# Kernel optimization log

Hardware: AMD Instinct MI355X
Metric: run time of the kernel (lower is better)

Reference implementation:

```python
import jax, jax.numpy as jnp
import numpy as np

IN_F = 4096
OUT_F = 4096

def setup_inputs() -> dict:
    key = jax.random.key(0)
    k1, k2 = jax.random.split(key)
    x = jax.random.normal(k1, (4, 2048, IN_F), dtype=jnp.float32)
    W = jax.random.normal(k2, (OUT_F, IN_F), dtype=jnp.float32) * (1.0 / np.sqrt(IN_F))
    return {"x": x, "W": W}

def reference(x, W):
    # per-tensor scale = mean |W|, clamped
    scale = jnp.maximum(jnp.mean(jnp.abs(W)), 1e-8)
    # pentanet: 5-level quantization {-2,-1,0,1,2}
    w_quant = jnp.clip(jnp.round(W / scale), -2.0, 2.0)
    # STE: forward uses quantized weights, gradient flows to W
    w_ste = jax.lax.stop_gradient(w_quant * scale - W) + W
    # F.linear: x @ w_ste.T -> [b, s, out]
    return jnp.einsum('bsi,oi->bso', x, w_ste)
```

## Files before the change

kernel.cpp:

```cpp
#include <hip/hip_runtime.h>
#include <cstdint>
#include <cstddef>

#define IN_F 4096
#define OUT_F 4096

typedef __attribute__((ext_vector_type(8))) short bf16x8;
typedef __attribute__((ext_vector_type(4))) float f32x4;

__device__ __forceinline__ ushort f32_bf16_rne(float f) {
    uint32_t u = __builtin_bit_cast(uint32_t, f);
    uint32_t r = (u + 0x7FFFu + ((u >> 16) & 1u)) >> 16;
    return (ushort)r;
}

__device__ __forceinline__ void gload_lds16(const void* g, void* l) {
    __builtin_amdgcn_global_load_lds(
        (const __attribute__((address_space(1))) uint32_t*)g,
        (__attribute__((address_space(3))) uint32_t*)l,
        16, 0, 0);
}

__device__ __forceinline__ void bar() {
    asm volatile("s_barrier" ::: "memory");
}

__global__ void reduce_abs1(const float* __restrict__ W, float* __restrict__ part) {
    __shared__ float sm[256];
    const int b = blockIdx.x, t = threadIdx.x;
    const float* p = W + (size_t)b * 4096;
    float s = 0.f;
#pragma unroll
    for (int j = 0; j < 16; ++j) s += fabsf(p[t + 256 * j]);
    sm[t] = s;
    __syncthreads();
    for (int w = 128; w > 0; w >>= 1) {
        if (t < w) sm[t] += sm[t + w];
        __syncthreads();
    }
    if (t == 0) part[b] = sm[0];
}

__global__ void reduce_abs2(const float* __restrict__ part, float* __restrict__ scale) {
    __shared__ float sm[256];
    const int t = threadIdx.x;
    float s = 0.f;
#pragma unroll
    for (int j = 0; j < 16; ++j) s += part[t + 256 * j];
    sm[t] = s;
    __syncthreads();
    for (int w = 128; w > 0; w >>= 1) {
        if (t < w) sm[t] += sm[t + w];
        __syncthreads();
    }
    if (t == 0) {
        float m = sm[0] / 16777216.0f;
        *scale = fmaxf(m, 1e-8f);
    }
}

__global__ void quantize_w(const float* __restrict__ W, ushort* __restrict__ wq,
                           const float* __restrict__ scale_p) {
    const int i = blockIdx.x * 256 + threadIdx.x;
    const float s = *scale_p;
    float4 v = ((const float4*)W)[i];
    float q0 = fminf(fmaxf(rintf(v.x / s), -2.f), 2.f);
    float q1 = fminf(fmaxf(rintf(v.y / s), -2.f), 2.f);
    float q2 = fminf(fmaxf(rintf(v.z / s), -2.f), 2.f);
    float q3 = fminf(fmaxf(rintf(v.w / s), -2.f), 2.f);
    ushort4 o;
    o.x = f32_bf16_rne(q0); o.y = f32_bf16_rne(q1);
    o.z = f32_bf16_rne(q2); o.w = f32_bf16_rne(q3);
    ((ushort4*)wq)[i] = o;
}

__global__ void cast_x(const float* __restrict__ X, ushort* __restrict__ xh) {
    const int i = blockIdx.x * 256 + threadIdx.x;
    float4 v = ((const float4*)X)[i];
    ushort4 o;
    o.x = f32_bf16_rne(v.x); o.y = f32_bf16_rne(v.y);
    o.z = f32_bf16_rne(v.z); o.w = f32_bf16_rne(v.w);
    ((ushort4*)xh)[i] = o;
}

#define BK 64
#define HT_BYTES 16384
#define BUF_BYTES 65536

__global__ __launch_bounds__(512, 2) void qgemm256(
        const ushort* __restrict__ Ab, const ushort* __restrict__ Bq,
        float* __restrict__ C, const float* __restrict__ scale_p,
        int M, int N, int K) {
    extern __shared__ __align__(16) char smem[];

    const int t = threadIdx.x;
    const int lane = t & 63;
    const int w = t >> 6;
    const int wr = w >> 2;
    const int wc = w & 3;
    const int bh = wc >> 1;

    const int MT = M >> 8;
    const int NTiles = N >> 8;
    int mt, nt;
    if (MT == 32 && NTiles == 16 && gridDim.x == 512) {
        const int x = blockIdx.x & 7;
        const int j = blockIdx.x >> 3;
        const int jr = j & 31;
        const int r = j >> 5;
        mt = (x & 3) * 8 + (jr & 7);
        nt = r * 8 + (x >> 2) * 4 + (jr >> 3);
    } else {
        const int nwg = gridDim.x;
        int wg = blockIdx.x;
        if ((nwg & 7) == 0) wg = (wg & 7) * (nwg >> 3) + (wg >> 3);
        mt = wg % MT; nt = wg / MT;
    }
    const int m0 = mt << 8;
    const int n0 = nt << 8;

    const int NT = K / BK;
    const int NS = NT * 4;

    int pre[2];
#pragma unroll
    for (int ks = 0; ks < 2; ++ks)
        pre[ks] = (lane & 15) * 128 +
                  (((ks * 64) + ((lane >> 4) * 16)) ^ ((lane & 7) << 4));

    auto do_stage = [&](int s) {
        if (s >= NS) return;
        const int kt = s >> 2, h = s & 3;
        const int k0 = kt * BK;
        char* bufbase = smem + (kt & 1) * BUF_BYTES;
        char* region;
        const ushort* gsrc;
        if (h < 2) {
            region = bufbase + h * HT_BYTES;
            gsrc = Ab + (size_t)(m0 + h * 128) * K + k0;
        } else {
            region = bufbase + 32768 + (h - 2) * HT_BYTES;
            gsrc = Bq + (size_t)(n0 + (h - 2) * 128) * K + k0;
        }
#pragma unroll
        for (int j = 0; j < 2; ++j) {
            int e = j * 4096 + t * 8;
            int r = e >> 6, c8 = (e >> 3) & 7;
            int srcc = (c8 ^ (r & 7)) * 8;
            gload_lds16(gsrc + (size_t)r * K + srcc, region + e * 2);
        }
    };

    f32x4 acc[8][4];
#pragma unroll
    for (int m = 0; m < 8; ++m)
#pragma unroll
        for (int n = 0; n < 4; ++n) acc[m][n] = (f32x4){0.f, 0.f, 0.f, 0.f};

    bf16x8 a0[4][2], a1[4][2], b01[2][2], b23[2][2];

    do_stage(0); do_stage(1); do_stage(2); do_stage(3);
    do_stage(4); do_stage(5); do_stage(6);
    asm volatile("s_waitcnt vmcnt(6)" ::: "memory");
    bar();
    {
        const char* aB = smem + wr * HT_BYTES;
        const char* bB = smem + 32768 + bh * HT_BYTES + (wc & 1) * 8192;
#pragma unroll
        for (int m = 0; m < 4; ++m)
#pragma unroll
            for (int ks = 0; ks < 2; ++ks)
                a0[m][ks] = *(const bf16x8*)(aB + m * 2048 + pre[ks]);
#pragma unroll
        for (int n = 0; n < 2; ++n)
#pragma unroll
            for (int ks = 0; ks < 2; ++ks)
                b01[n][ks] = *(const bf16x8*)(bB + n * 2048 + pre[ks]);
    }

    for (int kt = 0; kt < NT; ++kt) {
        const char* aB = smem + (kt & 1) * BUF_BYTES + wr * HT_BYTES;
        const char* bB = smem + (kt & 1) * BUF_BYTES + 32768 + bh * HT_BYTES +
                         (wc & 1) * 8192;
        const char* aBn = smem + ((kt + 1) & 1) * BUF_BYTES + wr * HT_BYTES;
        const char* bBn = smem + ((kt + 1) & 1) * BUF_BYTES + 32768 +
                          bh * HT_BYTES + (wc & 1) * 8192;

        do_stage(7 + 4 * kt);
        bar();
        __builtin_amdgcn_s_setprio(1);
#pragma unroll
        for (int m = 0; m < 4; ++m)
#pragma unroll
            for (int ks = 0; ks < 2; ++ks)
                a1[m][ks] = *(const bf16x8*)(aB + (m + 4) * 2048 + pre[ks]);
#pragma unroll
        for (int m = 0; m < 4; ++m)
#pragma unroll
            for (int n = 0; n < 2; ++n)
#pragma unroll
                for (int ks = 0; ks < 2; ++ks)
                    acc[m][n] = __builtin_amdgcn_mfma_f32_16x16x32_bf16(
                        a0[m][ks], b01[n][ks], acc[m][n], 0, 0, 0);
        __builtin_amdgcn_s_setprio(0);
        bar();

        do_stage(8 + 4 * kt);
        bar();
        __builtin_amdgcn_s_setprio(1);
#pragma unroll
        for (int n = 0; n < 2; ++n)
#pragma unroll
            for (int ks = 0; ks < 2; ++ks)
                b23[n][ks] = *(const bf16x8*)(bB + (n + 2) * 2048 + pre[ks]);
#pragma unroll
        for (int m = 0; m < 4; ++m)
#pragma unroll
            for (int n = 0; n < 2; ++n)
#pragma unroll
                for (int ks = 0; ks < 2; ++ks)
                    acc[m + 4][n] = __builtin_amdgcn_mfma_f32_16x16x32_bf16(
                        a1[m][ks], b01[n][ks], acc[m + 4][n], 0, 0, 0);
        __builtin_amdgcn_s_setprio(0);
        bar();

        do_stage(9 + 4 * kt);
        bar();
        __builtin_amdgcn_s_setprio(1);
#pragma unroll
        for (int m = 0; m < 4; ++m)
#pragma unroll
            for (int n = 0; n < 2; ++n)
#pragma unroll
                for (int ks = 0; ks < 2; ++ks)
                    acc[m][n + 2] = __builtin_amdgcn_mfma_f32_16x16x32_bf16(
                        a0[m][ks], b23[n][ks], acc[m][n + 2], 0, 0, 0);
        __builtin_amdgcn_s_setprio(0);
        bar();

        if (kt < NT - 2) {
            asm volatile("s_waitcnt vmcnt(4)" ::: "memory");
        } else {
            asm volatile("s_waitcnt vmcnt(0)" ::: "memory");
        }
        do_stage(10 + 4 * kt);
        bar();
        __builtin_amdgcn_s_setprio(1);
        if (kt + 1 < NT) {
#pragma unroll
            for (int m = 0; m < 4; ++m)
#pragma unroll
                for (int ks = 0; ks < 2; ++ks)
                    a0[m][ks] = *(const bf16x8*)(aBn + m * 2048 + pre[ks]);
#pragma unroll
            for (int n = 0; n < 2; ++n)
#pragma unroll
                for (int ks = 0; ks < 2; ++ks)
                    b01[n][ks] = *(const bf16x8*)(bBn + n * 2048 + pre[ks]);
        }
#pragma unroll
        for (int m = 0; m < 4; ++m)
#pragma unroll
            for (int n = 0; n < 2; ++n)
#pragma unroll
                for (int ks = 0; ks < 2; ++ks)
                    acc[m + 4][n + 2] = __builtin_amdgcn_mfma_f32_16x16x32_bf16(
                        a1[m][ks], b23[n][ks], acc[m + 4][n + 2], 0, 0, 0);
        __builtin_amdgcn_s_setprio(0);
        bar();
    }

    const float s = *scale_p;
#pragma unroll
    for (int m = 0; m < 8; ++m)
#pragma unroll
        for (int n = 0; n < 4; ++n) {
            const int col = n0 + wc * 64 + n * 16 + (lane & 15);
            const int rbase = m0 + wr * 128 + m * 16 + ((lane >> 4) << 2);
#pragma unroll
            for (int j = 0; j < 4; ++j)
                C[(size_t)(rbase + j) * N + col] = s * acc[m][n][j];
        }
}

template <bool ABF16>
__global__ __launch_bounds__(256) void qgemm(const void* __restrict__ Aptr,
                                             const ushort* __restrict__ Bq,
                                             float* __restrict__ C,
                                             const float* __restrict__ scale_p,
                                             int M, int N, int K) {
    __shared__ __align__(16) ushort sA[128 * 64];
    __shared__ __align__(16) ushort sB[128 * 64];

    const int t = threadIdx.x;
    const int lane = t & 63;
    const int w = t >> 6;
    const int wr = w >> 1, wc = w & 1;

    const int nwg = gridDim.x;
    int wg = blockIdx.x;
    if ((nwg & 7) == 0) wg = (wg & 7) * (nwg >> 3) + (wg >> 3);
    const int MT = M >> 7;
    const int mt = wg % MT;
    const int nt = wg / MT;
    const int m0 = mt * 128, n0 = nt * 128;

    const ushort* Ab = (const ushort*)Aptr;
    const float* Af = (const float*)Aptr;

    f32x4 zero = {0.f, 0.f, 0.f, 0.f};
    f32x4 acc[4][4];
#pragma unroll
    for (int m = 0; m < 4; ++m)
#pragma unroll
        for (int n = 0; n < 4; ++n) acc[m][n] = zero;

    for (int k0 = 0; k0 < K; k0 += 64) {
#pragma unroll
        for (int i = 0; i < 4; ++i) {
            int e = i * 2048 + t * 8;
            int r = e >> 6, c8 = (e >> 3) & 7;
            int srcc = (c8 ^ (r & 7)) * 8;
            gload_lds16(Bq + (size_t)(n0 + r) * K + (k0 + srcc), &sB[e]);
        }
        if constexpr (ABF16) {
#pragma unroll
            for (int i = 0; i < 4; ++i) {
                int e = i * 2048 + t * 8;
                int r = e >> 6, c8 = (e >> 3) & 7;
                int srcc = (c8 ^ (r & 7)) * 8;
                gload_lds16(Ab + (size_t)(m0 + r) * K + (k0 + srcc), &sA[e]);
            }
        } else {
#pragma unroll
            for (int i = 0; i < 4; ++i) {
                int e = i * 2048 + t * 8;
                int r = e >> 6, c = e & 63;
                const float* src = Af + (size_t)(m0 + r) * K + (k0 + c);
                float4 v0 = *(const float4*)src;
                float4 v1 = *(const float4*)(src + 4);
                bf16x8 pk;
                pk[0] = (short)f32_bf16_rne(v0.x); pk[1] = (short)f32_bf16_rne(v0.y);
                pk[2] = (short)f32_bf16_rne(v0.z); pk[3] = (short)f32_bf16_rne(v0.w);
                pk[4] = (short)f32_bf16_rne(v1.x); pk[5] = (short)f32_bf16_rne(v1.y);
                pk[6] = (short)f32_bf16_rne(v1.z); pk[7] = (short)f32_bf16_rne(v1.w);
                int byte = (r * 128 + c * 2) ^ ((r & 7) << 4);
                *(bf16x8*)((char*)sA + byte) = pk;
            }
        }
        __syncthreads();

#pragma unroll
        for (int ks = 0; ks < 2; ++ks) {
            const int kk = ks * 32 + ((lane >> 4) << 3);
            bf16x8 afr[4], bfr[4];
#pragma unroll
            for (int m = 0; m < 4; ++m) {
                int r = wr * 64 + m * 16 + (lane & 15);
                int byte = (r * 128 + kk * 2) ^ ((r & 7) << 4);
                afr[m] = *(const bf16x8*)((const char*)sA + byte);
            }
#pragma unroll
            for (int n = 0; n < 4; ++n) {
                int r = wc * 64 + n * 16 + (lane & 15);
                int byte = (r * 128 + kk * 2) ^ ((r & 7) << 4);
                bfr[n] = *(const bf16x8*)((const char*)sB + byte);
            }
#pragma unroll
            for (int m = 0; m < 4; ++m)
#pragma unroll
                for (int n = 0; n < 4; ++n)
                    acc[m][n] = __builtin_amdgcn_mfma_f32_16x16x32_bf16(
                        afr[m], bfr[n], acc[m][n], 0, 0, 0);
        }
        __syncthreads();
    }

    const float s = *scale_p;
#pragma unroll
    for (int m = 0; m < 4; ++m)
#pragma unroll
        for (int n = 0; n < 4; ++n) {
            const int col = n0 + wc * 64 + n * 16 + (lane & 15);
            const int rbase = m0 + wr * 64 + m * 16 + ((lane >> 4) << 2);
#pragma unroll
            for (int j = 0; j < 4; ++j)
                C[(size_t)(rbase + j) * N + col] = s * acc[m][n][j];
        }
}

__global__ void naive_qgemm(const float* __restrict__ X, const float* __restrict__ W,
                            float* __restrict__ out, const float* __restrict__ scale_p,
                            int M) {
    const int col = blockIdx.x * 256 + threadIdx.x;
    const int row = blockIdx.y;
    const float s = *scale_p;
    const float inv = 1.0f / s;
    const float* xr = X + (size_t)row * IN_F;
    const float* wrow = W + (size_t)col * IN_F;
    float acc = 0.f;
    for (int k = 0; k < IN_F; ++k) {
        float q = fminf(fmaxf(rintf(wrow[k] * inv), -2.f), 2.f);
        acc += xr[k] * q;
    }
    out[(size_t)row * OUT_F + col] = acc * s;
}

extern "C" void kernel_launch(void* const* d_in, const int* in_sizes, int n_in,
                              void* d_out, int out_size, void* d_ws, size_t ws_size,
                              hipStream_t stream) {
    const float* x = (const float*)d_in[0];
    const float* W = (const float*)d_in[1];
    float* out = (float*)d_out;
    const int M = in_sizes[0] / IN_F;
    const int K = IN_F, N = OUT_F;

    char* ws = (char*)d_ws;
    const size_t OFF_PART = 512;
    const size_t OFF_WQ = OFF_PART + 4096 * sizeof(float);
    const size_t WQ_BYTES = (size_t)N * K * sizeof(ushort);
    const size_t OFF_XH = OFF_WQ + WQ_BYTES;
    const size_t XH_BYTES = (size_t)M * K * sizeof(ushort);
    float* scale = (float*)(ws + 0);
    float* part = (float*)(ws + OFF_PART);
    ushort* wq = (ushort*)(ws + OFF_WQ);
    ushort* xh = (ushort*)(ws + OFF_XH);

    if (ws_size < OFF_WQ) return;

    reduce_abs1<<<4096, 256, 0, stream>>>(W, part);
    reduce_abs2<<<1, 256, 0, stream>>>(part, scale);

    if (ws_size >= OFF_XH + XH_BYTES && (M % 256) == 0 && (N % 256) == 0) {
        quantize_w<<<(N * K / 4) / 256, 256, 0, stream>>>(W, wq, scale);
        cast_x<<<(M * K / 4) / 256, 256, 0, stream>>>(x, xh);
        (void)hipFuncSetAttribute((const void*)qgemm256,
                                  hipFuncAttributeMaxDynamicSharedMemorySize,
                                  131072);
        qgemm256<<<(M / 256) * (N / 256), 512, 131072, stream>>>(
            xh, wq, out, scale, M, N, K);
    } else if (ws_size >= OFF_XH + XH_BYTES) {
        quantize_w<<<(N * K / 4) / 256, 256, 0, stream>>>(W, wq, scale);
        cast_x<<<(M * K / 4) / 256, 256, 0, stream>>>(x, xh);
        qgemm<true><<<(M / 128) * (N / 128), 256, 0, stream>>>(xh, wq, out, scale, M, N, K);
    } else if (ws_size >= OFF_WQ + WQ_BYTES) {
        quantize_w<<<(N * K / 4) / 256, 256, 0, stream>>>(W, wq, scale);
        qgemm<false><<<(M / 128) * (N / 128), 256, 0, stream>>>(x, wq, out, scale, M, N, K);
    } else {
        naive_qgemm<<<dim3(N / 256, M), 256, 0, stream>>>(x, W, out, scale, M);
    }
}
```

Measured before the change: 328.6 us.

## Collapse four-phase GEMM pipeline into one load stage per k-tile

```diff
diff --git a/kernel.cpp b/kernel.cpp
--- a/kernel.cpp
+++ b/kernel.cpp
@@ -84,7 +84,6 @@
 }
 
 #define BK 64
-#define HT_BYTES 16384
 #define BUF_BYTES 65536
 
 __global__ __launch_bounds__(512, 2) void qgemm256(
@@ -120,7 +119,6 @@
     const int n0 = nt << 8;
 
     const int NT = K / BK;
-    const int NS = NT * 4;
 
     int pre[2];
 #pragma unroll
@@ -128,28 +126,32 @@
         pre[ks] = (lane & 15) * 128 +
                   (((ks * 64) + ((lane >> 4) * 16)) ^ ((lane & 7) << 4));
 
-    auto do_stage = [&](int s) {
-        if (s >= NS) return;
-        const int kt = s >> 2, h = s & 3;
-        const int k0 = kt * BK;
-        char* bufbase = smem + (kt & 1) * BUF_BYTES;
-        char* region;
-        const ushort* gsrc;
-        if (h < 2) {
-            region = bufbase + h * HT_BYTES;
-            gsrc = Ab + (size_t)(m0 + h * 128) * K + k0;
-        } else {
-            region = bufbase + 32768 + (h - 2) * HT_BYTES;
-            gsrc = Bq + (size_t)(n0 + (h - 2) * 128) * K + k0;
-        }
-#pragma unroll
-        for (int j = 0; j < 2; ++j) {
-            int e = j * 4096 + t * 8;
-            int r = e >> 6, c8 = (e >> 3) & 7;
-            int srcc = (c8 ^ (r & 7)) * 8;
-            gload_lds16(gsrc + (size_t)r * K + srcc, region + e * 2);
-        }
+    const int rowA = t >> 3;
+    const int colsw = ((t & 7) ^ ((t >> 3) & 7)) << 3;
+    const ushort* gA0 = Ab + (size_t)(m0 + rowA) * K + colsw;
+    const ushort* gA1 = Ab + (size_t)(m0 + 128 + rowA) * K + colsw;
+    const ushort* gB0 = Bq + (size_t)(n0 + rowA) * K + colsw;
+    const ushort* gB1 = Bq + (size_t)(n0 + 128 + rowA) * K + colsw;
+    const size_t jrow = (size_t)64 * K;
+    char* lb = smem + t * 16;
+
+    auto stA = [&](uint32_t par) {
+        gload_lds16(gA0,        lb + par);
+        gload_lds16(gA0 + jrow, lb + par + 8192);
+        gload_lds16(gA1,        lb + par + 16384);
+        gload_lds16(gA1 + jrow, lb + par + 24576);
+        gA0 += 64; gA1 += 64;
     };
+    auto stB = [&](uint32_t par) {
+        gload_lds16(gB0,        lb + par + 32768);
+        gload_lds16(gB0 + jrow, lb + par + 40960);
+        gload_lds16(gB1,        lb + par + 49152);
+        gload_lds16(gB1 + jrow, lb + par + 57344);
+        gB0 += 64; gB1 += 64;
+    };
+
+    const char* aBbase = smem + wr * 16384;
+    const char* bBbase = smem + 32768 + bh * 16384 + (wc & 1) * 8192;
 
     f32x4 acc[8][4];
 #pragma unroll
@@ -159,41 +161,36 @@
 
     bf16x8 a0[4][2], a1[4][2], b01[2][2], b23[2][2];
 
-    do_stage(0); do_stage(1); do_stage(2); do_stage(3);
-    do_stage(4); do_stage(5); do_stage(6);
-    asm volatile("s_waitcnt vmcnt(6)" ::: "memory");
+    stA(0); stB(0);
+    stA(BUF_BYTES); stB(BUF_BYTES);
+    asm volatile("s_waitcnt vmcnt(8)" ::: "memory");
     bar();
-    {
-        const char* aB = smem + wr * HT_BYTES;
-        const char* bB = smem + 32768 + bh * HT_BYTES + (wc & 1) * 8192;
-#pragma unroll
-        for (int m = 0; m < 4; ++m)
-#pragma unroll
-            for (int ks = 0; ks < 2; ++ks)
-                a0[m][ks] = *(const bf16x8*)(aB + m * 2048 + pre[ks]);
-#pragma unroll
-        for (int n = 0; n < 2; ++n)
-#pragma unroll
-            for (int ks = 0; ks < 2; ++ks)
-                b01[n][ks] = *(const bf16x8*)(bB + n * 2048 + pre[ks]);
-    }
+#pragma unroll
+    for (int m = 0; m < 4; ++m)
+#pragma unroll
+        for (int ks = 0; ks < 2; ++ks) {
+            a0[m][ks] = *(const bf16x8*)(aBbase + m * 2048 + pre[ks]);
+            a1[m][ks] = *(const bf16x8*)(aBbase + (m + 4) * 2048 + pre[ks]);
+        }
+#pragma unroll
+    for (int n = 0; n < 2; ++n)
+#pragma unroll
+        for (int ks = 0; ks < 2; ++ks) {
+            b01[n][ks] = *(const bf16x8*)(bBbase + n * 2048 + pre[ks]);
+            b23[n][ks] = *(const bf16x8*)(bBbase + (n + 2) * 2048 + pre[ks]);
+        }
 
     for (int kt = 0; kt < NT; ++kt) {
-        const char* aB = smem + (kt & 1) * BUF_BYTES + wr * HT_BYTES;
-        const char* bB = smem + (kt & 1) * BUF_BYTES + 32768 + bh * HT_BYTES +
-                         (wc & 1) * 8192;
-        const char* aBn = smem + ((kt + 1) & 1) * BUF_BYTES + wr * HT_BYTES;
-        const char* bBn = smem + ((kt + 1) & 1) * BUF_BYTES + 32768 +
-                          bh * HT_BYTES + (wc & 1) * 8192;
-
-        do_stage(7 + 4 * kt);
+        const uint32_t cur = (uint32_t)(kt & 1) * BUF_BYTES;
+        const uint32_t nxt = cur ^ BUF_BYTES;
+        const char* aBn = aBbase + nxt;
+        const char* bBn = bBbase + nxt;
+
+        asm volatile("s_waitcnt vmcnt(0)" ::: "memory");
+        if (kt + 2 < NT) { stA(cur); stB(cur); }
         bar();
+
         __builtin_amdgcn_s_setprio(1);
-#pragma unroll
-        for (int m = 0; m < 4; ++m)
-#pragma unroll
-            for (int ks = 0; ks < 2; ++ks)
-                a1[m][ks] = *(const bf16x8*)(aB + (m + 4) * 2048 + pre[ks]);
 #pragma unroll
         for (int m = 0; m < 4; ++m)
 #pragma unroll
@@ -202,17 +199,6 @@
                 for (int ks = 0; ks < 2; ++ks)
                     acc[m][n] = __builtin_amdgcn_mfma_f32_16x16x32_bf16(
                         a0[m][ks], b01[n][ks], acc[m][n], 0, 0, 0);
-        __builtin_amdgcn_s_setprio(0);
-        bar();
-
-        do_stage(8 + 4 * kt);
-        bar();
-        __builtin_amdgcn_s_setprio(1);
-#pragma unroll
-        for (int n = 0; n < 2; ++n)
-#pragma unroll
-            for (int ks = 0; ks < 2; ++ks)
-                b23[n][ks] = *(const bf16x8*)(bB + (n + 2) * 2048 + pre[ks]);
 #pragma unroll
         for (int m = 0; m < 4; ++m)
 #pragma unroll
@@ -221,12 +207,6 @@
                 for (int ks = 0; ks < 2; ++ks)
                     acc[m + 4][n] = __builtin_amdgcn_mfma_f32_16x16x32_bf16(
                         a1[m][ks], b01[n][ks], acc[m + 4][n], 0, 0, 0);
-        __builtin_amdgcn_s_setprio(0);
-        bar();
-
-        do_stage(9 + 4 * kt);
-        bar();
-        __builtin_amdgcn_s_setprio(1);
 #pragma unroll
         for (int m = 0; m < 4; ++m)
 #pragma unroll
@@ -235,29 +215,6 @@
                 for (int ks = 0; ks < 2; ++ks)
                     acc[m][n + 2] = __builtin_amdgcn_mfma_f32_16x16x32_bf16(
                         a0[m][ks], b23[n][ks], acc[m][n + 2], 0, 0, 0);
-        __builtin_amdgcn_s_setprio(0);
-        bar();
-
-        if (kt < NT - 2) {
-            asm volatile("s_waitcnt vmcnt(4)" ::: "memory");
-        } else {
-            asm volatile("s_waitcnt vmcnt(0)" ::: "memory");
-        }
-        do_stage(10 + 4 * kt);
-        bar();
-        __builtin_amdgcn_s_setprio(1);
-        if (kt + 1 < NT) {
-#pragma unroll
-            for (int m = 0; m < 4; ++m)
-#pragma unroll
-                for (int ks = 0; ks < 2; ++ks)
-                    a0[m][ks] = *(const bf16x8*)(aBn + m * 2048 + pre[ks]);
-#pragma unroll
-            for (int n = 0; n < 2; ++n)
-#pragma unroll
-                for (int ks = 0; ks < 2; ++ks)
-                    b01[n][ks] = *(const bf16x8*)(bBn + n * 2048 + pre[ks]);
-        }
 #pragma unroll
         for (int m = 0; m < 4; ++m)
 #pragma unroll
@@ -266,7 +223,24 @@
                 for (int ks = 0; ks < 2; ++ks)
                     acc[m + 4][n + 2] = __builtin_amdgcn_mfma_f32_16x16x32_bf16(
                         a1[m][ks], b23[n][ks], acc[m + 4][n + 2], 0, 0, 0);
+        if (kt + 1 < NT) {
+#pragma unroll
+            for (int m = 0; m < 4; ++m)
+#pragma unroll
+                for (int ks = 0; ks < 2; ++ks) {
+                    a0[m][ks] = *(const bf16x8*)(aBn + m * 2048 + pre[ks]);
+                    a1[m][ks] = *(const bf16x8*)(aBn + (m + 4) * 2048 + pre[ks]);
+                }
+#pragma unroll
+            for (int n = 0; n < 2; ++n)
+#pragma unroll
+                for (int ks = 0; ks < 2; ++ks) {
+                    b01[n][ks] = *(const bf16x8*)(bBn + n * 2048 + pre[ks]);
+                    b23[n][ks] = *(const bf16x8*)(bBn + (n + 2) * 2048 + pre[ks]);
+                }
+        }
         __builtin_amdgcn_s_setprio(0);
+        asm volatile("s_waitcnt lgkmcnt(0)" ::: "memory");
         bar();
     }
 
```

Measured after the change: 313.9 us. 4.5% less time.
